# Performance work log

Hardware: AMD Instinct MI355X
Metric: run time of the kernel (lower is better)

Reference implementation:

```python
import jax, jax.numpy as jnp
import numpy as np

NUM_TOKENS = 16384  # batch 4 * seq 4096
D_MODEL = 4096
NUM_EXPERTS = 64
TOP_K = 2  # hardcoded in the original forward


def setup_inputs() -> dict:
    key = jax.random.key(0)
    kx, kw, kb = jax.random.split(key, 3)
    x = jax.random.normal(kx, (NUM_TOKENS, D_MODEL), dtype=jnp.float32)
    # router linear params (lecun_normal-ish scale)
    W = jax.random.normal(kw, (D_MODEL, NUM_EXPERTS), dtype=jnp.float32) / np.sqrt(D_MODEL)
    b = jnp.zeros((NUM_EXPERTS,), dtype=jnp.float32)
    return {"x": x, "W": W, "b": b}


def reference(x, W, b):
    # router logits: skinny GEMM [N, D] @ [D, E]
    router_logits = jnp.einsum("nd,de->ne", x, W) + b
    router_probs = jax.nn.softmax(router_logits, axis=-1)
    top_k_probs, top_k_indices = jax.lax.top_k(router_probs, TOP_K)
    # renormalize the selected probabilities to sum to 1
    top_k_probs = top_k_probs / jnp.sum(top_k_probs, axis=-1, keepdims=True)
    return top_k_probs, top_k_indices
```

## Files before the change

### kernel.cpp

```cpp
#include <hip/hip_runtime.h>
#include <math.h>

#define NTOK   16384
#define DMODEL 4096
#define NEXP   64
#define WAVES  16
#define TOKS   64
#define KPW    (DMODEL / WAVES)
#define KT     32
#define NCHUNK (KPW / KT)

#define LD4(p) (*(const float4*)(p))

#define FMA_K(vv, kk) do {                                   \
    const float* wr = wbase + (size_t)(kk) * NEXP;           \
    _Pragma("unroll")                                        \
    for (int e = 0; e < NEXP; ++e)                           \
        acc[e] = fmaf(wr[e], (vv), acc[e]);                  \
} while (0)

#define DO4(q, kc) do {                                      \
    FMA_K((q).x, (kc) + 0);                                  \
    FMA_K((q).y, (kc) + 1);                                  \
    FMA_K((q).z, (kc) + 2);                                  \
    FMA_K((q).w, (kc) + 3);                                  \
} while (0)

__global__ __launch_bounds__(WAVES * 64, 4)
void router_kernel(const float* __restrict__ x,
                   const float* __restrict__ W,
                   const float* __restrict__ b,
                   float* __restrict__ out)
{
    __shared__ float la[NEXP * TOKS];
    __shared__ float lb[NEXP * TOKS];

    const int tid  = threadIdx.x;
    const int lane = tid & 63;
    const int wid  = tid >> 6;
    const int t0   = blockIdx.x * TOKS;

    const int kb = __builtin_amdgcn_readfirstlane(wid * KPW);

    const float* wbase = W + (size_t)kb * NEXP;
    const float* xrow  = x + (size_t)(t0 + lane) * DMODEL + kb;

    float acc[NEXP];
#pragma unroll
    for (int e = 0; e < NEXP; ++e) acc[e] = 0.f;

    float4 c0 = LD4(xrow + 0),  c1 = LD4(xrow + 4),
           c2 = LD4(xrow + 8),  c3 = LD4(xrow + 12),
           c4 = LD4(xrow + 16), c5 = LD4(xrow + 20),
           c6 = LD4(xrow + 24), c7 = LD4(xrow + 28);

    for (int c = 0; c < NCHUNK - 1; ++c) {
        const float* nx = xrow + (c + 1) * KT;
        float4 n0 = LD4(nx + 0),  n1 = LD4(nx + 4),
               n2 = LD4(nx + 8),  n3 = LD4(nx + 12),
               n4 = LD4(nx + 16), n5 = LD4(nx + 20),
               n6 = LD4(nx + 24), n7 = LD4(nx + 28);
        const int kc = c * KT;
        DO4(c0, kc + 0);  DO4(c1, kc + 4);
        DO4(c2, kc + 8);  DO4(c3, kc + 12);
        DO4(c4, kc + 16); DO4(c5, kc + 20);
        DO4(c6, kc + 24); DO4(c7, kc + 28);
        c0 = n0; c1 = n1; c2 = n2; c3 = n3;
        c4 = n4; c5 = n5; c6 = n6; c7 = n7;
    }
    {
        const int kc = (NCHUNK - 1) * KT;
        DO4(c0, kc + 0);  DO4(c1, kc + 4);
        DO4(c2, kc + 8);  DO4(c3, kc + 12);
        DO4(c4, kc + 16); DO4(c5, kc + 20);
        DO4(c6, kc + 24); DO4(c7, kc + 28);
    }

    {
        float* dst = (wid < 8) ? la : lb;
        const int slot = wid & 7;
        for (int r = 0; r < 8; ++r) {
            if (slot == r) {
                if (r == 0) {
#pragma unroll
                    for (int e = 0; e < NEXP; ++e) dst[e * TOKS + lane] = acc[e];
                } else {
#pragma unroll
                    for (int e = 0; e < NEXP; ++e) dst[e * TOKS + lane] += acc[e];
                }
            }
            __syncthreads();
        }
    }

    if (wid == 0) {
        const int t = t0 + lane;
        float l[NEXP];
        float m = -INFINITY;
#pragma unroll
        for (int e = 0; e < NEXP; ++e) {
            l[e] = la[e * TOKS + lane] + lb[e * TOKS + lane] + b[e];
            m = fmaxf(m, l[e]);
        }
        float Z = 0.f;
#pragma unroll
        for (int e = 0; e < NEXP; ++e) {
            l[e] = expf(l[e] - m);
            Z += l[e];
        }
        float p1 = -1.f, p2 = -1.f;
        int i1 = 0, i2 = 0;
#pragma unroll
        for (int e = 0; e < NEXP; ++e) {
            const float p = l[e] / Z;
            if (p > p1) { p2 = p1; i2 = i1; p1 = p; i1 = e; }
            else if (p > p2) { p2 = p; i2 = e; }
        }
        const float s = p1 + p2;
        out[2 * t]     = p1 / s;
        out[2 * t + 1] = p2 / s;
        out[2 * NTOK + 2 * t]     = (float)i1;
        out[2 * NTOK + 2 * t + 1] = (float)i2;
    }
}

extern "C" void kernel_launch(void* const* d_in, const int* in_sizes, int n_in,
                              void* d_out, int out_size, void* d_ws, size_t ws_size,
                              hipStream_t stream) {
    const float* x = (const float*)d_in[0];
    const float* W = (const float*)d_in[1];
    const float* b = (const float*)d_in[2];
    float* out = (float*)d_out;
    router_kernel<<<dim3(NTOK / TOKS), dim3(WAVES * 64), 0, stream>>>(x, W, b, out);
}
```

Measured before the change: 485.5 us.

## Split K across blocks and finalize softmax/top-k in separate kernel

Partitions the reduction dimension across two grid slices, using 8-wave blocks instead of 16. Each block writes partial logits to workspace, and a second kernel sums the partials, adds bias and runs softmax plus top-2. This doubles the block count with smaller blocks to raise occupancy and scheduling flexibility. The cost is an extra launch and a workspace round trip of 2x64x16384 floats.

```diff
diff --git a/kernel.cpp b/kernel.cpp
--- a/kernel.cpp
+++ b/kernel.cpp
@@ -4,9 +4,10 @@
 #define NTOK   16384
 #define DMODEL 4096
 #define NEXP   64
-#define WAVES  16
+#define KSPLIT 2
+#define WAVES  8
 #define TOKS   64
-#define KPW    (DMODEL / WAVES)
+#define KPW    (DMODEL / (KSPLIT * WAVES))
 #define KT     32
 #define NCHUNK (KPW / KT)
 
@@ -27,10 +28,9 @@
 } while (0)
 
 __global__ __launch_bounds__(WAVES * 64, 4)
-void router_kernel(const float* __restrict__ x,
-                   const float* __restrict__ W,
-                   const float* __restrict__ b,
-                   float* __restrict__ out)
+void router_partial(const float* __restrict__ x,
+                    const float* __restrict__ W,
+                    float* __restrict__ ws)
 {
     __shared__ float la[NEXP * TOKS];
     __shared__ float lb[NEXP * TOKS];
@@ -39,8 +39,9 @@
     const int lane = tid & 63;
     const int wid  = tid >> 6;
     const int t0   = blockIdx.x * TOKS;
+    const int kp   = blockIdx.y;
 
-    const int kb = __builtin_amdgcn_readfirstlane(wid * KPW);
+    const int kb = __builtin_amdgcn_readfirstlane((kp * WAVES + wid) * KPW);
 
     const float* wbase = W + (size_t)kb * NEXP;
     const float* xrow  = x + (size_t)(t0 + lane) * DMODEL + kb;
@@ -77,9 +78,9 @@
     }
 
     {
-        float* dst = (wid < 8) ? la : lb;
-        const int slot = wid & 7;
-        for (int r = 0; r < 8; ++r) {
+        float* dst = (wid < 4) ? la : lb;
+        const int slot = wid & 3;
+        for (int r = 0; r < 4; ++r) {
             if (slot == r) {
                 if (r == 0) {
 #pragma unroll
@@ -93,35 +94,52 @@
         }
     }
 
-    if (wid == 0) {
-        const int t = t0 + lane;
-        float l[NEXP];
-        float m = -INFINITY;
+    {
+        const int e0 = wid * 8;
 #pragma unroll
-        for (int e = 0; e < NEXP; ++e) {
-            l[e] = la[e * TOKS + lane] + lb[e * TOKS + lane] + b[e];
-            m = fmaxf(m, l[e]);
+        for (int i = 0; i < 8; ++i) {
+            const int e = e0 + i;
+            ws[((size_t)kp * NEXP + e) * NTOK + t0 + lane] =
+                la[e * TOKS + lane] + lb[e * TOKS + lane];
         }
-        float Z = 0.f;
+    }
+}
+
+__global__ __launch_bounds__(64)
+void router_finalize(const float* __restrict__ ws,
+                     const float* __restrict__ b,
+                     float* __restrict__ out)
+{
+    const int t = blockIdx.x * 64 + threadIdx.x;
+
+    float l[NEXP];
+    float m = -INFINITY;
 #pragma unroll
-        for (int e = 0; e < NEXP; ++e) {
-            l[e] = expf(l[e] - m);
-            Z += l[e];
-        }
-        float p1 = -1.f, p2 = -1.f;
-        int i1 = 0, i2 = 0;
+    for (int e = 0; e < NEXP; ++e) {
+        l[e] = ws[(size_t)e * NTOK + t]
+             + ws[((size_t)NEXP + e) * NTOK + t]
+             + b[e];
+        m = fmaxf(m, l[e]);
+    }
+    float Z = 0.f;
 #pragma unroll
-        for (int e = 0; e < NEXP; ++e) {
-            const float p = l[e] / Z;
-            if (p > p1) { p2 = p1; i2 = i1; p1 = p; i1 = e; }
-            else if (p > p2) { p2 = p; i2 = e; }
-        }
-        const float s = p1 + p2;
-        out[2 * t]     = p1 / s;
-        out[2 * t + 1] = p2 / s;
-        out[2 * NTOK + 2 * t]     = (float)i1;
-        out[2 * NTOK + 2 * t + 1] = (float)i2;
+    for (int e = 0; e < NEXP; ++e) {
+        l[e] = expf(l[e] - m);
+        Z += l[e];
     }
+    float p1 = -1.f, p2 = -1.f;
+    int i1 = 0, i2 = 0;
+#pragma unroll
+    for (int e = 0; e < NEXP; ++e) {
+        const float p = l[e] / Z;
+        if (p > p1) { p2 = p1; i2 = i1; p1 = p; i1 = e; }
+        else if (p > p2) { p2 = p; i2 = e; }
+    }
+    const float s = p1 + p2;
+    out[2 * t]     = p1 / s;
+    out[2 * t + 1] = p2 / s;
+    out[2 * NTOK + 2 * t]     = (float)i1;
+    out[2 * NTOK + 2 * t + 1] = (float)i2;
 }
 
 extern "C" void kernel_launch(void* const* d_in, const int* in_sizes, int n_in,
@@ -131,5 +149,8 @@
     const float* W = (const float*)d_in[1];
     const float* b = (const float*)d_in[2];
     float* out = (float*)d_out;
-    router_kernel<<<dim3(NTOK / TOKS), dim3(WAVES * 64), 0, stream>>>(x, W, b, out);
+    float* ws  = (float*)d_ws;
+
+    router_partial<<<dim3(NTOK / TOKS, KSPLIT), dim3(WAVES * 64), 0, stream>>>(x, W, ws);
+    router_finalize<<<dim3(NTOK / 64), dim3(64), 0, stream>>>(ws, b, out);
 }
```

New measurement: 497.0 us. 1.02x slower.
